# Kernel optimization log

Hardware: AMD Instinct MI355X
Metric: run time of the kernel (lower is better)

## Reference

```python
import jax, jax.numpy as jnp
from jax import lax
import numpy as np

B = 4096
L = 20  # nb_latents


def conv2d(x, w, b, stride, pad):
    y = lax.conv_general_dilated(x, w, (stride, stride), [(pad, pad), (pad, pad)],
                                 dimension_numbers=('NCHW', 'OIHW', 'NCHW'))
    return y + b[None, :, None, None]


def deconv2d(x, w, b, stride, pad):
    # w has PyTorch ConvTranspose2d layout [Cin, Cout, kh, kw]
    k = w.shape[2]
    w2 = jnp.flip(w, (2, 3)).transpose(1, 0, 2, 3)  # -> [Cout, Cin, kh, kw]
    y = lax.conv_general_dilated(x, w2, (1, 1), [(k - 1 - pad,) * 2] * 2,
                                 lhs_dilation=(stride, stride),
                                 dimension_numbers=('NCHW', 'OIHW', 'NCHW'))
    return y + b[None, :, None, None]


def setup_inputs() -> dict:
    key = jax.random.key(0)
    ks = jax.random.split(key, 16)

    def W(k, shape, fan_in, scale=1.0):
        return (jax.random.normal(k, shape, jnp.float32) * (scale / np.sqrt(fan_in))).astype(jnp.float32)

    z = lambda n: jnp.zeros((n,), jnp.float32)
    return {
        'x': jax.random.uniform(ks[0], (B, 1, 28, 28), jnp.float32),
        'eps': jax.random.normal(ks[1], (B, L), jnp.float32),
        'w_c1': W(ks[2], (32, 1, 4, 4), 16), 'b_c1': z(32),
        'w_c2': W(ks[3], (32, 32, 4, 4), 512), 'b_c2': z(32),
        'w_c3': W(ks[4], (64, 32, 3, 3), 288), 'b_c3': z(64),
        'w_fc1': W(ks[5], (256, 1024), 1024), 'b_fc1': z(256),
        'w_mu': W(ks[6], (L, 256), 256), 'b_mu': z(L),
        # small scale + negative bias keeps the 100-step exp(logvar) recursion in fp32 range
        'w_ls': W(ks[7], (L, 256), 256, 0.1), 'b_ls': jnp.full((L,), -2.0, jnp.float32),
        'w_fc2': W(ks[8], (256, L), L), 'b_fc2': z(256),
        'w_fc3': W(ks[9], (1024, 256), 256), 'b_fc3': z(1024),
        'w_d1': W(ks[10], (64, 32, 3, 3), 576), 'b_d1': z(32),
        'w_d2': W(ks[11], (32, 32, 4, 4), 512), 'b_d2': z(32),
        'w_d3': W(ks[12], (32, 1, 4, 4), 512), 'b_d3': z(1),
    }


def reference(x, eps, w_c1, b_c1, w_c2, b_c2, w_c3, b_c3, w_fc1, b_fc1,
              w_mu, b_mu, w_ls, b_ls, w_fc2, b_fc2, w_fc3, b_fc3,
              w_d1, b_d1, w_d2, b_d2, w_d3, b_d3):
    # ---- encoder ----
    h = jax.nn.relu(conv2d(x, w_c1, b_c1, 2, 1))   # [B,32,14,14]
    h = jax.nn.relu(conv2d(h, w_c2, b_c2, 2, 1))   # [B,32,7,7]
    h = jax.nn.relu(conv2d(h, w_c3, b_c3, 2, 1))   # [B,64,4,4]
    h = jax.nn.relu(h.reshape(-1, 64 * 4 * 4) @ w_fc1.T + b_fc1)
    mu = h @ w_mu.T + b_mu          # [B,L]
    logvar = h @ w_ls.T + b_ls      # [B,L]

    # ---- reversing: 100 gradient-ascent steps on KLD (eval-mode reparameterize) ----
    # KLD = -0.5 * sum(1 + ls - mu^2 - exp(ls))  =>  dKLD/dmu = mu, dKLD/dls = 0.5*(exp(ls)-1)
    lr = 0.1
    def step(c, _):
        m, s = c
        return (m + lr * m, s + lr * 0.5 * (jnp.exp(s) - 1.0)), None
    (mu_r, ls_r), _ = lax.scan(step, (mu, logvar), None, length=100)
    zlat = eps * jnp.exp(0.5 * ls_r) + mu_r

    # ---- decoder ----
    d = jax.nn.relu(zlat @ w_fc2.T + b_fc2)
    d = jax.nn.relu(d @ w_fc3.T + b_fc3).reshape(-1, 64, 4, 4)
    d = jax.nn.relu(deconv2d(d, w_d1, b_d1, 2, 1))       # [B,32,7,7]
    d = jax.nn.relu(deconv2d(d, w_d2, b_d2, 2, 1))       # [B,32,14,14]
    x_hat = jax.nn.sigmoid(deconv2d(d, w_d3, b_d3, 2, 1))  # [B,1,28,28]
    return x_hat, mu, logvar
```

## Files before the change

### kernel.cpp

```cpp
#include <hip/hip_runtime.h>
#include <math.h>

#define BATCH 4096

__device__ __forceinline__ void dot4a(float& acc, const float4 v, const float4 wt) {
    acc = fmaf(v.x, wt.x, acc);
    acc = fmaf(v.y, wt.y, acc);
    acc = fmaf(v.z, wt.z, acc);
    acc = fmaf(v.w, wt.w, acc);
}

__global__ __launch_bounds__(256) void tr_kernel(
    const float* __restrict__ w_c2, const float* __restrict__ w_c3,
    const float* __restrict__ w_d1, const float* __restrict__ w_d2,
    const float* __restrict__ w_d3,
    float* __restrict__ wt2, float* __restrict__ wt3,
    float* __restrict__ wtd1, float* __restrict__ wtd2, float* __restrict__ wtd3)
{
    int i = blockIdx.x * 256 + threadIdx.x;
    if (i < 16384) {
        int ci = i & 31, tap = (i >> 5) & 15, co = i >> 9;
        wt2[i] = w_c2[(co * 32 + ci) * 16 + tap];
    }
    if (i < 18432) {
        int ci = i & 31, r = i >> 5, tap = r % 9, co = r / 9;
        wt3[i] = w_c3[(co * 32 + ci) * 9 + tap];
    }
    if (i < 18432) {
        int ci = i & 63, r = i >> 6, tap = r % 9, co = r / 9;
        wtd1[i] = w_d1[(ci * 32 + co) * 9 + tap];
    }
    if (i < 16384) {
        int ci = i & 31, tap = (i >> 5) & 15, co = i >> 9;
        wtd2[i] = w_d2[(ci * 32 + co) * 16 + tap];
    }
    if (i < 512) {
        int ci = i & 31, tap = i >> 5;
        wtd3[i] = w_d3[ci * 16 + tap];
    }
}

__global__ __launch_bounds__(256, 3) void enc_kernel(
    const float* __restrict__ x,
    const float* __restrict__ w_c1, const float* __restrict__ b_c1,
    const float* __restrict__ wt2, const float* __restrict__ b_c2,
    const float* __restrict__ wt3, const float* __restrict__ b_c3,
    float* __restrict__ h3out)
{
    __shared__ __align__(16) float buf[12708];
    float* s_h1 = buf;
    float* s_h3 = buf;
    float* s_x  = buf + 9216;
    float* s_h2 = buf + 10116;

    const int n = blockIdx.x, tid = threadIdx.x;
    const int wv = __builtin_amdgcn_readfirstlane((int)(tid >> 6));
    const int lane = tid & 63;
    const int co0 = wv * 8;

    {
        float4* z1 = (float4*)buf;
        #pragma unroll
        for (int i = tid; i < 2304; i += 256) z1[i] = make_float4(0.f, 0.f, 0.f, 0.f);
        float4* z2 = (float4*)(buf + 10116);
        for (int i = tid; i < 648; i += 256) z2[i] = make_float4(0.f, 0.f, 0.f, 0.f);
        for (int i = tid; i < 30; i += 256) { s_x[i] = 0.f; s_x[870 + i] = 0.f; }
        for (int i = tid; i < 28; i += 256) { s_x[(i + 1) * 30] = 0.f; s_x[(i + 1) * 30 + 29] = 0.f; }
        for (int i = tid; i < 784; i += 256) {
            int iy = i / 28, ix = i - iy * 28;
            s_x[(iy + 1) * 30 + ix + 1] = x[(size_t)n * 784 + i];
        }
    }
    __syncthreads();

    {
        const int poff = lane & 15, pr = lane >> 4;
        const int ca = co0 + pr * 2;
        float w1a[16], w1b[16];
        #pragma unroll
        for (int k = 0; k < 4; ++k) {
            *(float4*)&w1a[4 * k] = *(const float4*)(w_c1 + ca * 16 + 4 * k);
            *(float4*)&w1b[4 * k] = *(const float4*)(w_c1 + (ca + 1) * 16 + 4 * k);
        }
        const float ba = b_c1[ca], bb = b_c1[ca + 1];
        for (int t = 0; t < 13; ++t) {
            int pos = poff + 16 * t;
            bool val = pos < 196;
            int p = val ? pos : 0;
            int oy = p / 14, ox = p - oy * 14;
            const float* bp = s_x + (2 * oy) * 30 + 2 * ox;
            float a0 = ba, a1 = bb;
            #pragma unroll
            for (int ky = 0; ky < 4; ++ky)
                #pragma unroll
                for (int kx = 0; kx < 4; ++kx) {
                    float v = bp[ky * 30 + kx];
                    a0 = fmaf(v, w1a[ky * 4 + kx], a0);
                    a1 = fmaf(v, w1b[ky * 4 + kx], a1);
                }
            if (val)
                *(float2*)(s_h1 + ((oy + 1) * 16 + ox + 1) * 36 + ca) =
                    make_float2(fmaxf(a0, 0.f), fmaxf(a1, 0.f));
        }
    }
    __syncthreads();

    {
        const int parity = lane & 1, pr = (lane >> 1) & 3, cig = lane >> 3;
        const int ca = co0 + pr * 2;
        float4 w2a[16], w2b[16];
        #pragma unroll
        for (int t = 0; t < 16; ++t) {
            w2a[t] = *(const float4*)(wt2 + (ca * 16 + t) * 32 + cig * 4);
            w2b[t] = *(const float4*)(wt2 + ((ca + 1) * 16 + t) * 32 + cig * 4);
        }
        const float ba = b_c2[ca], bb = b_c2[ca + 1];
        for (int t = 0; t < 25; ++t) {
            int pos = parity + 2 * t;
            bool val = pos < 49;
            int p = val ? pos : 0;
            int oy = p / 7, ox = p - oy * 7;
            const float* bp = s_h1 + ((2 * oy) * 16 + 2 * ox) * 36 + cig * 4;
            float a0 = 0.f, a1 = 0.f;
            #pragma unroll
            for (int ky = 0; ky < 4; ++ky)
                #pragma unroll
                for (int kx = 0; kx < 4; ++kx) {
                    float4 v = *(const float4*)(bp + (ky * 16 + kx) * 36);
                    dot4a(a0, v, w2a[ky * 4 + kx]);
                    dot4a(a1, v, w2b[ky * 4 + kx]);
                }
            a0 += __shfl_xor(a0, 8);  a1 += __shfl_xor(a1, 8);
            a0 += __shfl_xor(a0, 16); a1 += __shfl_xor(a1, 16);
            a0 += __shfl_xor(a0, 32); a1 += __shfl_xor(a1, 32);
            if (cig == 0 && val)
                *(float2*)(s_h2 + ((oy + 1) * 9 + ox + 1) * 32 + ca) =
                    make_float2(fmaxf(a0 + ba, 0.f), fmaxf(a1 + bb, 0.f));
        }
    }
    __syncthreads();

    {
        const int pr = lane & 7, cig = lane >> 3;
        const int ca = wv * 16 + pr * 2;
        float4 w3a[9], w3b[9];
        #pragma unroll
        for (int t = 0; t < 9; ++t) {
            w3a[t] = *(const float4*)(wt3 + (ca * 9 + t) * 32 + cig * 4);
            w3b[t] = *(const float4*)(wt3 + ((ca + 1) * 9 + t) * 32 + cig * 4);
        }
        const float ba = b_c3[ca], bb = b_c3[ca + 1];
        #pragma unroll 2
        for (int pos = 0; pos < 16; ++pos) {
            int oy = pos >> 2, ox = pos & 3;
            const float* bp = s_h2 + ((2 * oy) * 9 + 2 * ox) * 32 + cig * 4;
            float a0 = 0.f, a1 = 0.f;
            #pragma unroll
            for (int ky = 0; ky < 3; ++ky)
                #pragma unroll
                for (int kx = 0; kx < 3; ++kx) {
                    float4 v = *(const float4*)(bp + (ky * 9 + kx) * 32);
                    dot4a(a0, v, w3a[ky * 3 + kx]);
                    dot4a(a1, v, w3b[ky * 3 + kx]);
                }
            a0 += __shfl_xor(a0, 8);  a1 += __shfl_xor(a1, 8);
            a0 += __shfl_xor(a0, 16); a1 += __shfl_xor(a1, 16);
            a0 += __shfl_xor(a0, 32); a1 += __shfl_xor(a1, 32);
            if (cig == 0) {
                s_h3[ca * 16 + pos] = fmaxf(a0 + ba, 0.f);
                s_h3[(ca + 1) * 16 + pos] = fmaxf(a1 + bb, 0.f);
            }
        }
    }
    __syncthreads();
    for (int i = tid; i < 1024; i += 256) h3out[(size_t)n * 1024 + i] = s_h3[i];
}

template <bool RELU>
__global__ __launch_bounds__(256) void gemm_nt(
    const float* __restrict__ A, const float* __restrict__ W,
    const float* __restrict__ bias, float* __restrict__ C,
    int M, int N, int K)
{
    __shared__ float As[16][65];
    __shared__ float Ws[16][65];
    const int tid = threadIdx.x;
    const int col0 = blockIdx.x * 64;
    const int row0 = blockIdx.y * 64;
    const int tx = tid & 15, ty = tid >> 4;
    const int lr = tid >> 2, lc = (tid & 3) * 4;
    float acc[4][4] = {};

    for (int k0 = 0; k0 < K; k0 += 16) {
        float4 av = *(const float4*)(A + (size_t)(row0 + lr) * K + k0 + lc);
        float4 wv = *(const float4*)(W + (size_t)(col0 + lr) * K + k0 + lc);
        As[lc + 0][lr] = av.x; As[lc + 1][lr] = av.y; As[lc + 2][lr] = av.z; As[lc + 3][lr] = av.w;
        Ws[lc + 0][lr] = wv.x; Ws[lc + 1][lr] = wv.y; Ws[lc + 2][lr] = wv.z; Ws[lc + 3][lr] = wv.w;
        __syncthreads();
        #pragma unroll
        for (int kk = 0; kk < 16; ++kk) {
            float a[4], b[4];
            #pragma unroll
            for (int i = 0; i < 4; ++i) a[i] = As[kk][ty * 4 + i];
            #pragma unroll
            for (int j = 0; j < 4; ++j) b[j] = Ws[kk][tx * 4 + j];
            #pragma unroll
            for (int i = 0; i < 4; ++i)
                #pragma unroll
                for (int j = 0; j < 4; ++j)
                    acc[i][j] = fmaf(a[i], b[j], acc[i][j]);
        }
        __syncthreads();
    }
    #pragma unroll
    for (int i = 0; i < 4; ++i) {
        int row = row0 + ty * 4 + i;
        float* cp = C + (size_t)row * N + col0 + tx * 4;
        float4 v;
        v.x = acc[i][0] + bias[col0 + tx * 4 + 0];
        v.y = acc[i][1] + bias[col0 + tx * 4 + 1];
        v.z = acc[i][2] + bias[col0 + tx * 4 + 2];
        v.w = acc[i][3] + bias[col0 + tx * 4 + 3];
        if (RELU) {
            v.x = fmaxf(v.x, 0.f); v.y = fmaxf(v.y, 0.f);
            v.z = fmaxf(v.z, 0.f); v.w = fmaxf(v.w, 0.f);
        }
        *(float4*)cp = v;
    }
}

__global__ __launch_bounds__(256) void muls_kernel(
    const float* __restrict__ h,
    const float* __restrict__ w_mu, const float* __restrict__ b_mu,
    const float* __restrict__ w_ls, const float* __restrict__ b_ls,
    float* __restrict__ mu_out, float* __restrict__ ls_out)
{
    int idx = blockIdx.x * 256 + threadIdx.x;
    if (idx >= BATCH * 40) return;
    int i = idx / 40, j = idx % 40;
    bool is_mu = j < 20;
    int jj = is_mu ? j : j - 20;
    const float* wrow = is_mu ? (w_mu + jj * 256) : (w_ls + jj * 256);
    float acc = is_mu ? b_mu[jj] : b_ls[jj];
    const float4* hp = (const float4*)(h + (size_t)i * 256);
    const float4* wp = (const float4*)wrow;
    #pragma unroll 8
    for (int k = 0; k < 64; ++k) {
        float4 hv = hp[k], wv = wp[k];
        acc = fmaf(hv.x, wv.x, acc);
        acc = fmaf(hv.y, wv.y, acc);
        acc = fmaf(hv.z, wv.z, acc);
        acc = fmaf(hv.w, wv.w, acc);
    }
    (is_mu ? mu_out : ls_out)[i * 20 + jj] = acc;
}

__global__ __launch_bounds__(256) void rev_kernel(
    const float* __restrict__ mu, const float* __restrict__ ls,
    const float* __restrict__ eps, float* __restrict__ z)
{
    int idx = blockIdx.x * 256 + threadIdx.x;
    if (idx >= BATCH * 20) return;
    double m = (double)mu[idx];
    double s = (double)ls[idx];
    #pragma unroll 4
    for (int t = 0; t < 100; ++t) {
        m += 0.1 * m;
        s += 0.05 * (exp(s) - 1.0);
    }
    z[idx] = (float)((double)eps[idx] * exp(0.5 * s) + m);
}

__global__ __launch_bounds__(256) void fc2_kernel(
    const float* __restrict__ z, const float* __restrict__ w, const float* __restrict__ b,
    float* __restrict__ out)
{
    int idx = blockIdx.x * 256 + threadIdx.x;
    int i = idx >> 8, j = idx & 255;
    float acc = b[j];
    const float* zp = z + i * 20;
    const float* wp = w + j * 20;
    #pragma unroll
    for (int k = 0; k < 20; ++k) acc = fmaf(zp[k], wp[k], acc);
    out[idx] = fmaxf(acc, 0.f);
}

__global__ __launch_bounds__(256, 3) void dec_kernel(
    const float* __restrict__ hin,
    const float* __restrict__ wtd1, const float* __restrict__ b_d1,
    const float* __restrict__ wtd2, const float* __restrict__ b_d2,
    const float* __restrict__ wtd3, const float* __restrict__ b_d3,
    float* __restrict__ xhat)
{
    __shared__ __align__(16) float dbuf[12896];
    float* s_d2   = dbuf;
    float* s_d1   = dbuf + 9216;
    float* s_in   = dbuf + 11808;
    float* s_part = dbuf + 11808;

    const int n = blockIdx.x, tid = threadIdx.x;
    const int wv = __builtin_amdgcn_readfirstlane((int)(tid >> 6));
    const int lane = tid & 63;
    const int co0 = wv * 8;

    {
        float4* z1 = (float4*)dbuf;
        #pragma unroll
        for (int i = tid; i < 2952; i += 256) z1[i] = make_float4(0.f, 0.f, 0.f, 0.f);
        for (int t = tid; t < 1024; t += 256) {
            int c = t & 63, p = t >> 6;
            s_in[p * 68 + c] = hin[(size_t)n * 1024 + c * 16 + p];
        }
    }
    __syncthreads();

    {
        const int pr = lane & 3, cig = lane >> 2;
        const int ca = co0 + pr * 2;
        float4 wa[9], wb[9];
        #pragma unroll
        for (int t = 0; t < 9; ++t) {
            wa[t] = *(const float4*)(wtd1 + (ca * 9 + t) * 64 + cig * 4);
            wb[t] = *(const float4*)(wtd1 + ((ca + 1) * 9 + t) * 64 + cig * 4);
        }
        const float ba = b_d1[ca], bb = b_d1[ca + 1];
        #pragma unroll
        for (int py = 0; py < 2; ++py) {
            #pragma unroll
            for (int px = 0; px < 2; ++px) {
                const int ny = 4 - py, nx = 4 - px;
                for (int sy = 0; sy < ny; ++sy) {
                    for (int sx = 0; sx < nx; ++sx) {
                        float a0 = 0.f, a1 = 0.f;
                        #pragma unroll
                        for (int a = 0; a <= 1; ++a) {
                            if (a == 1 && py == 0) continue;
                            int ky = py ? (a ? 2 : 0) : 1;
                            int iy = py ? (a ? sy : sy + 1) : sy;
                            #pragma unroll
                            for (int b = 0; b <= 1; ++b) {
                                if (b == 1 && px == 0) continue;
                                int kx = px ? (b ? 2 : 0) : 1;
                                int ix = px ? (b ? sx : sx + 1) : sx;
                                float4 v = *(const float4*)(s_in + (iy * 4 + ix) * 68 + cig * 4);
                                int tp = ky * 3 + kx;
                                dot4a(a0, v, wa[tp]);
                                dot4a(a1, v, wb[tp]);
                            }
                        }
                        a0 += __shfl_xor(a0, 4);  a1 += __shfl_xor(a1, 4);
                        a0 += __shfl_xor(a0, 8);  a1 += __shfl_xor(a1, 8);
                        a0 += __shfl_xor(a0, 16); a1 += __shfl_xor(a1, 16);
                        a0 += __shfl_xor(a0, 32); a1 += __shfl_xor(a1, 32);
                        if (cig == 0) {
                            int oy = 2 * sy + py, ox = 2 * sx + px;
                            *(float2*)(s_d1 + ((oy + 1) * 9 + ox + 1) * 32 + ca) =
                                make_float2(fmaxf(a0 + ba, 0.f), fmaxf(a1 + bb, 0.f));
                        }
                    }
                }
            }
        }
    }
    __syncthreads();

    {
        const int soff = lane & 1, pr = (lane >> 1) & 3, cig = lane >> 3;
        const int ca = co0 + pr * 2;
        float4 wa[16], wb[16];
        #pragma unroll
        for (int t = 0; t < 16; ++t) {
            wa[t] = *(const float4*)(wtd2 + (ca * 16 + t) * 32 + cig * 4);
            wb[t] = *(const float4*)(wtd2 + ((ca + 1) * 16 + t) * 32 + cig * 4);
        }
        const float ba = b_d2[ca], bb = b_d2[ca + 1];
        for (int t = 0; t < 25; ++t) {
            int spos = soff + 2 * t;
            bool val = spos < 49;
            int sp = val ? spos : 0;
            int sy = sp / 7, sx = sp - sy * 7;
            const float* bp = s_d1 + (sy * 9 + sx) * 32 + cig * 4;
            #pragma unroll
            for (int py = 0; py < 2; ++py) {
                float4 va[2][3];
                #pragma unroll
                for (int l = 0; l < 2; ++l)
                    #pragma unroll
                    for (int b = 0; b < 3; ++b)
                        va[l][b] = *(const float4*)(bp + ((l + py) * 9 + b) * 32);
                #pragma unroll
                for (int px = 0; px < 2; ++px) {
                    float a0 = 0.f, a1 = 0.f;
                    #pragma unroll
                    for (int a2 = 0; a2 < 2; ++a2) {
                        int ky = py ? (a2 ? 2 : 0) : (a2 ? 3 : 1);
                        int l = 1 - a2;
                        #pragma unroll
                        for (int b2 = 0; b2 < 2; ++b2) {
                            int kx = px ? (b2 ? 2 : 0) : (b2 ? 3 : 1);
                            int m = px ? (2 - b2) : (1 - b2);
                            int tp = ky * 4 + kx;
                            float4 v = va[l][m];
                            dot4a(a0, v, wa[tp]);
                            dot4a(a1, v, wb[tp]);
                        }
                    }
                    a0 += __shfl_xor(a0, 8);  a1 += __shfl_xor(a1, 8);
                    a0 += __shfl_xor(a0, 16); a1 += __shfl_xor(a1, 16);
                    a0 += __shfl_xor(a0, 32); a1 += __shfl_xor(a1, 32);
                    if (cig == 0 && val) {
                        int oy = 2 * sy + py, ox = 2 * sx + px;
                        *(float2*)(s_d2 + ((oy + 1) * 16 + ox + 1) * 36 + ca) =
                            make_float2(fmaxf(a0 + ba, 0.f), fmaxf(a1 + bb, 0.f));
                    }
                }
            }
        }
    }
    __syncthreads();

    {
        const int ci0 = wv * 8;
        const float bd3 = b_d3[0];
        #pragma unroll
        for (int py = 0; py < 2; ++py) {
            #pragma unroll
            for (int px = 0; px < 2; ++px) {
                float w3r[2][2][8];
                #pragma unroll
                for (int a = 0; a < 2; ++a) {
                    int ky = py ? (a ? 2 : 0) : (a ? 3 : 1);
                    #pragma unroll
                    for (int b = 0; b < 2; ++b) {
                        int kx = px ? (b ? 2 : 0) : (b ? 3 : 1);
                        *(float4*)(w3r[a][b])     = *(const float4*)(wtd3 + (ky * 4 + kx) * 32 + ci0);
                        *(float4*)(w3r[a][b] + 4) = *(const float4*)(wtd3 + (ky * 4 + kx) * 32 + ci0 + 4);
                    }
                }
                for (int t = 0; t < 4; ++t) {
                    int spos = t * 64 + lane;
                    bool val = spos < 196;
                    int sp = val ? spos : 0;
                    int sy = sp / 14, sx = sp - sy * 14;
                    const float* bp = s_d2 + ((sy + py) * 16 + sx + px) * 36 + ci0;
                    float acc = 0.f;
                    #pragma unroll
                    for (int a = 0; a < 2; ++a) {
                        #pragma unroll
                        for (int b = 0; b < 2; ++b) {
                            const float* vp = bp + ((1 - a) * 16 + (1 - b)) * 36;
                            float4 v0 = *(const float4*)(vp);
                            float4 v1 = *(const float4*)(vp + 4);
                            acc = fmaf(v0.x, w3r[a][b][0], acc);
                            acc = fmaf(v0.y, w3r[a][b][1], acc);
                            acc = fmaf(v0.z, w3r[a][b][2], acc);
                            acc = fmaf(v0.w, w3r[a][b][3], acc);
                            acc = fmaf(v1.x, w3r[a][b][4], acc);
                            acc = fmaf(v1.y, w3r[a][b][5], acc);
                            acc = fmaf(v1.z, w3r[a][b][6], acc);
                            acc = fmaf(v1.w, w3r[a][b][7], acc);
                        }
                    }
                    if (val) s_part[wv * 196 + sp] = acc;
                }
                __syncthreads();
                if (tid < 196) {
                    float s = s_part[tid] + s_part[196 + tid] + s_part[392 + tid] + s_part[588 + tid];
                    int sy = tid / 14, sx = tid - sy * 14;
                    xhat[(size_t)n * 784 + (2 * sy + py) * 28 + 2 * sx + px] =
                        1.f / (1.f + expf(-(s + bd3)));
                }
                __syncthreads();
            }
        }
    }
}

extern "C" void kernel_launch(void* const* d_in, const int* in_sizes, int n_in,
                              void* d_out, int out_size, void* d_ws, size_t ws_size,
                              hipStream_t stream) {
    const float* x     = (const float*)d_in[0];
    const float* eps   = (const float*)d_in[1];
    const float* w_c1  = (const float*)d_in[2];
    const float* b_c1  = (const float*)d_in[3];
    const float* w_c2  = (const float*)d_in[4];
    const float* b_c2  = (const float*)d_in[5];
    const float* w_c3  = (const float*)d_in[6];
    const float* b_c3  = (const float*)d_in[7];
    const float* w_fc1 = (const float*)d_in[8];
    const float* b_fc1 = (const float*)d_in[9];
    const float* w_mu  = (const float*)d_in[10];
    const float* b_mu  = (const float*)d_in[11];
    const float* w_ls  = (const float*)d_in[12];
    const float* b_ls  = (const float*)d_in[13];
    const float* w_fc2 = (const float*)d_in[14];
    const float* b_fc2 = (const float*)d_in[15];
    const float* w_fc3 = (const float*)d_in[16];
    const float* b_fc3 = (const float*)d_in[17];
    const float* w_d1  = (const float*)d_in[18];
    const float* b_d1  = (const float*)d_in[19];
    const float* w_d2  = (const float*)d_in[20];
    const float* b_d2  = (const float*)d_in[21];
    const float* w_d3  = (const float*)d_in[22];
    const float* b_d3  = (const float*)d_in[23];

    float* out = (float*)d_out;
    float* x_hat  = out;
    float* mu_out = out + 4096 * 784;
    float* ls_out = mu_out + 4096 * 20;

    float* buf1 = (float*)d_ws;
    float* buf2 = buf1 + 4096 * 1024;
    float* zlat = buf1;
    float* wt2  = buf2 + 4096 * 256;
    float* wt3  = wt2 + 16384;
    float* wtd1 = wt3 + 18432;
    float* wtd2 = wtd1 + 18432;
    float* wtd3 = wtd2 + 16384;

    tr_kernel<<<72, 256, 0, stream>>>(w_c2, w_c3, w_d1, w_d2, w_d3, wt2, wt3, wtd1, wtd2, wtd3);
    enc_kernel<<<BATCH, 256, 0, stream>>>(x, w_c1, b_c1, wt2, b_c2, wt3, b_c3, buf1);
    gemm_nt<true><<<dim3(256 / 64, BATCH / 64), 256, 0, stream>>>(buf1, w_fc1, b_fc1, buf2, BATCH, 256, 1024);
    muls_kernel<<<(BATCH * 40) / 256, 256, 0, stream>>>(buf2, w_mu, b_mu, w_ls, b_ls, mu_out, ls_out);
    rev_kernel<<<(BATCH * 20) / 256, 256, 0, stream>>>(mu_out, ls_out, eps, zlat);
    fc2_kernel<<<BATCH, 256, 0, stream>>>(zlat, w_fc2, b_fc2, buf2);
    gemm_nt<true><<<dim3(1024 / 64, BATCH / 64), 256, 0, stream>>>(buf2, w_fc3, b_fc3, buf1, BATCH, 1024, 256);
    dec_kernel<<<BATCH, 256, 0, stream>>>(buf1, wtd1, b_d1, wtd2, b_d2, wtd3, b_d3, x_hat);
}
```

Before: 787.7 us.

## Fuse mu/logvar projection with reversal loop and restructure decoder deconvolutions

Merges the mu/logvar matvec and the 100-step reversal recursion into one kernel, and moves the logvar recursion from double to float exp. The decoder is reorganised: deconv1/deconv2 assign 4 output channels per lane with fewer shuffle reductions and register-held weights. The final deconv is split into a per-pixel 32-to-16-tap partial product followed by a gather-sum with sigmoid, which removes the per-phase barriers. Float exp in the recursion may change numerics slightly, and the larger per-lane weight arrays raise register pressure.

```diff
diff --git a/kernel.cpp b/kernel.cpp
--- a/kernel.cpp
+++ b/kernel.cpp
@@ -229,46 +229,38 @@
     }
 }
 
-__global__ __launch_bounds__(256) void muls_kernel(
+__global__ __launch_bounds__(256) void mulsrev_kernel(
     const float* __restrict__ h,
     const float* __restrict__ w_mu, const float* __restrict__ b_mu,
     const float* __restrict__ w_ls, const float* __restrict__ b_ls,
-    float* __restrict__ mu_out, float* __restrict__ ls_out)
-{
-    int idx = blockIdx.x * 256 + threadIdx.x;
-    if (idx >= BATCH * 40) return;
-    int i = idx / 40, j = idx % 40;
-    bool is_mu = j < 20;
-    int jj = is_mu ? j : j - 20;
-    const float* wrow = is_mu ? (w_mu + jj * 256) : (w_ls + jj * 256);
-    float acc = is_mu ? b_mu[jj] : b_ls[jj];
-    const float4* hp = (const float4*)(h + (size_t)i * 256);
-    const float4* wp = (const float4*)wrow;
-    #pragma unroll 8
-    for (int k = 0; k < 64; ++k) {
-        float4 hv = hp[k], wv = wp[k];
-        acc = fmaf(hv.x, wv.x, acc);
-        acc = fmaf(hv.y, wv.y, acc);
-        acc = fmaf(hv.z, wv.z, acc);
-        acc = fmaf(hv.w, wv.w, acc);
-    }
-    (is_mu ? mu_out : ls_out)[i * 20 + jj] = acc;
-}
-
-__global__ __launch_bounds__(256) void rev_kernel(
-    const float* __restrict__ mu, const float* __restrict__ ls,
-    const float* __restrict__ eps, float* __restrict__ z)
+    const float* __restrict__ eps,
+    float* __restrict__ mu_out, float* __restrict__ ls_out, float* __restrict__ z)
 {
     int idx = blockIdx.x * 256 + threadIdx.x;
     if (idx >= BATCH * 20) return;
-    double m = (double)mu[idx];
-    double s = (double)ls[idx];
+    int i = idx / 20, j = idx - i * 20;
+    const float4* hp = (const float4*)(h + (size_t)i * 256);
+    const float4* mp = (const float4*)(w_mu + j * 256);
+    const float4* lp = (const float4*)(w_ls + j * 256);
+    float am = b_mu[j], al = b_ls[j];
+    #pragma unroll 8
+    for (int k = 0; k < 64; ++k) {
+        float4 hv = hp[k], mv = mp[k], lv = lp[k];
+        am = fmaf(hv.x, mv.x, am); al = fmaf(hv.x, lv.x, al);
+        am = fmaf(hv.y, mv.y, am); al = fmaf(hv.y, lv.y, al);
+        am = fmaf(hv.z, mv.z, am); al = fmaf(hv.z, lv.z, al);
+        am = fmaf(hv.w, mv.w, am); al = fmaf(hv.w, lv.w, al);
+    }
+    mu_out[idx] = am;
+    ls_out[idx] = al;
+    double m = (double)am;
+    float s = al;
     #pragma unroll 4
     for (int t = 0; t < 100; ++t) {
         m += 0.1 * m;
-        s += 0.05 * (exp(s) - 1.0);
-    }
-    z[idx] = (float)((double)eps[idx] * exp(0.5 * s) + m);
+        s += 0.05f * (expf(s) - 1.f);
+    }
+    z[idx] = fmaf(eps[idx], expf(0.5f * s), (float)m);
 }
 
 __global__ __launch_bounds__(256) void fc2_kernel(
@@ -292,11 +284,11 @@
     const float* __restrict__ wtd3, const float* __restrict__ b_d3,
     float* __restrict__ xhat)
 {
-    __shared__ __align__(16) float dbuf[12896];
-    float* s_d2   = dbuf;
-    float* s_d1   = dbuf + 9216;
-    float* s_in   = dbuf + 11808;
-    float* s_part = dbuf + 11808;
+    __shared__ __align__(16) float dbuf[11060];
+    float* s_d2 = dbuf;
+    float* s_d1 = dbuf + 7056;
+    float* s_in = dbuf + 9972;
+    float* sP   = dbuf + 7056;
 
     const int n = blockIdx.x, tid = threadIdx.x;
     const int wv = __builtin_amdgcn_readfirstlane((int)(tid >> 6));
@@ -304,9 +296,8 @@
     const int co0 = wv * 8;
 
     {
-        float4* z1 = (float4*)dbuf;
-        #pragma unroll
-        for (int i = tid; i < 2952; i += 256) z1[i] = make_float4(0.f, 0.f, 0.f, 0.f);
+        float4* z1 = (float4*)(dbuf + 7056);
+        for (int i = tid; i < 729; i += 256) z1[i] = make_float4(0.f, 0.f, 0.f, 0.f);
         for (int t = tid; t < 1024; t += 256) {
             int c = t & 63, p = t >> 6;
             s_in[p * 68 + c] = hin[(size_t)n * 1024 + c * 16 + p];
@@ -315,162 +306,194 @@
     __syncthreads();
 
     {
-        const int pr = lane & 3, cig = lane >> 2;
-        const int ca = co0 + pr * 2;
-        float4 wa[9], wb[9];
-        #pragma unroll
-        for (int t = 0; t < 9; ++t) {
-            wa[t] = *(const float4*)(wtd1 + (ca * 9 + t) * 64 + cig * 4);
-            wb[t] = *(const float4*)(wtd1 + ((ca + 1) * 9 + t) * 64 + cig * 4);
-        }
-        const float ba = b_d1[ca], bb = b_d1[ca + 1];
+        const int cig = lane & 7, pq = (lane >> 3) & 1, poff = lane >> 4;
+        const int ci0 = cig * 8;
+        const int ca = co0 + pq * 4;
+        float bd[4];
+        #pragma unroll
+        for (int u = 0; u < 4; ++u) bd[u] = b_d1[ca + u];
+
         #pragma unroll
         for (int py = 0; py < 2; ++py) {
             #pragma unroll
             for (int px = 0; px < 2; ++px) {
                 const int ny = 4 - py, nx = 4 - px;
-                for (int sy = 0; sy < ny; ++sy) {
-                    for (int sx = 0; sx < nx; ++sx) {
-                        float a0 = 0.f, a1 = 0.f;
+                const int P = ny * nx;
+                const int na = py ? 2 : 1, nb = px ? 2 : 1;
+                float4 wd[4][2][2][2];
+                #pragma unroll
+                for (int u = 0; u < 4; ++u)
+                    #pragma unroll
+                    for (int a = 0; a < 2; ++a) {
+                        if (a >= na) continue;
                         #pragma unroll
-                        for (int a = 0; a <= 1; ++a) {
-                            if (a == 1 && py == 0) continue;
+                        for (int b = 0; b < 2; ++b) {
+                            if (b >= nb) continue;
                             int ky = py ? (a ? 2 : 0) : 1;
-                            int iy = py ? (a ? sy : sy + 1) : sy;
+                            int kx = px ? (b ? 2 : 0) : 1;
+                            const float* wp = wtd1 + ((ca + u) * 9 + ky * 3 + kx) * 64 + ci0;
+                            wd[u][a][b][0] = *(const float4*)(wp);
+                            wd[u][a][b][1] = *(const float4*)(wp + 4);
+                        }
+                    }
+                const int niter = (P + 3) >> 2;
+                for (int it = 0; it < niter; ++it) {
+                    int pidx = it * 4 + poff;
+                    bool act = pidx < P;
+                    int p = act ? pidx : 0;
+                    int sy = p / nx, sx = p - sy * nx;
+                    float acc[4] = {};
+                    #pragma unroll
+                    for (int a = 0; a < 2; ++a) {
+                        if (a >= na) continue;
+                        int iy = py ? (a ? sy : sy + 1) : sy;
+                        #pragma unroll
+                        for (int b = 0; b < 2; ++b) {
+                            if (b >= nb) continue;
+                            int ix = px ? (b ? sx : sx + 1) : sx;
+                            const float* bp = s_in + (iy * 4 + ix) * 68 + ci0;
+                            float4 v0 = *(const float4*)(bp);
+                            float4 v1 = *(const float4*)(bp + 4);
                             #pragma unroll
-                            for (int b = 0; b <= 1; ++b) {
-                                if (b == 1 && px == 0) continue;
-                                int kx = px ? (b ? 2 : 0) : 1;
-                                int ix = px ? (b ? sx : sx + 1) : sx;
-                                float4 v = *(const float4*)(s_in + (iy * 4 + ix) * 68 + cig * 4);
-                                int tp = ky * 3 + kx;
-                                dot4a(a0, v, wa[tp]);
-                                dot4a(a1, v, wb[tp]);
+                            for (int u = 0; u < 4; ++u) {
+                                dot4a(acc[u], v0, wd[u][a][b][0]);
+                                dot4a(acc[u], v1, wd[u][a][b][1]);
                             }
                         }
-                        a0 += __shfl_xor(a0, 4);  a1 += __shfl_xor(a1, 4);
-                        a0 += __shfl_xor(a0, 8);  a1 += __shfl_xor(a1, 8);
-                        a0 += __shfl_xor(a0, 16); a1 += __shfl_xor(a1, 16);
-                        a0 += __shfl_xor(a0, 32); a1 += __shfl_xor(a1, 32);
-                        if (cig == 0) {
-                            int oy = 2 * sy + py, ox = 2 * sx + px;
-                            *(float2*)(s_d1 + ((oy + 1) * 9 + ox + 1) * 32 + ca) =
-                                make_float2(fmaxf(a0 + ba, 0.f), fmaxf(a1 + bb, 0.f));
-                        }
                     }
-                }
-            }
-        }
-    }
-    __syncthreads();
-
-    {
-        const int soff = lane & 1, pr = (lane >> 1) & 3, cig = lane >> 3;
-        const int ca = co0 + pr * 2;
-        float4 wa[16], wb[16];
-        #pragma unroll
-        for (int t = 0; t < 16; ++t) {
-            wa[t] = *(const float4*)(wtd2 + (ca * 16 + t) * 32 + cig * 4);
-            wb[t] = *(const float4*)(wtd2 + ((ca + 1) * 16 + t) * 32 + cig * 4);
-        }
-        const float ba = b_d2[ca], bb = b_d2[ca + 1];
-        for (int t = 0; t < 25; ++t) {
-            int spos = soff + 2 * t;
-            bool val = spos < 49;
-            int sp = val ? spos : 0;
+                    #pragma unroll
+                    for (int u = 0; u < 4; ++u) {
+                        acc[u] += __shfl_xor(acc[u], 1);
+                        acc[u] += __shfl_xor(acc[u], 2);
+                        acc[u] += __shfl_xor(acc[u], 4);
+                    }
+                    if (cig == 0 && act) {
+                        int oy = 2 * sy + py, ox = 2 * sx + px;
+                        float4 o;
+                        o.x = fmaxf(acc[0] + bd[0], 0.f);
+                        o.y = fmaxf(acc[1] + bd[1], 0.f);
+                        o.z = fmaxf(acc[2] + bd[2], 0.f);
+                        o.w = fmaxf(acc[3] + bd[3], 0.f);
+                        *(float4*)(s_d1 + ((oy + 1) * 9 + ox + 1) * 36 + ca) = o;
+                    }
+                }
+            }
+        }
+    }
+    __syncthreads();
+
+    {
+        const int cig = lane & 3, pq = (lane >> 2) & 1;
+        const int py = (lane >> 3) & 1, px = (lane >> 4) & 1, poff = lane >> 5;
+        const int ci0 = cig * 8;
+        const int ca = co0 + pq * 4;
+        float4 w2[4][2][2][2];
+        float bd[4];
+        #pragma unroll
+        for (int u = 0; u < 4; ++u) {
+            bd[u] = b_d2[ca + u];
+            #pragma unroll
+            for (int a = 0; a < 2; ++a)
+                #pragma unroll
+                for (int b = 0; b < 2; ++b) {
+                    int ky = py ? (a ? 2 : 0) : (a ? 3 : 1);
+                    int kx = px ? (b ? 2 : 0) : (b ? 3 : 1);
+                    const float* wp = wtd2 + ((ca + u) * 16 + ky * 4 + kx) * 32 + ci0;
+                    w2[u][a][b][0] = *(const float4*)(wp);
+                    w2[u][a][b][1] = *(const float4*)(wp + 4);
+                }
+        }
+        for (int it = 0; it < 25; ++it) {
+            int pidx = it * 2 + poff;
+            bool act = pidx < 49;
+            int sp = act ? pidx : 0;
             int sy = sp / 7, sx = sp - sy * 7;
-            const float* bp = s_d1 + (sy * 9 + sx) * 32 + cig * 4;
-            #pragma unroll
-            for (int py = 0; py < 2; ++py) {
-                float4 va[2][3];
-                #pragma unroll
-                for (int l = 0; l < 2; ++l)
+            float acc[4] = {};
+            #pragma unroll
+            for (int a = 0; a < 2; ++a) {
+                int iy = py ? (a ? sy : sy + 1) : (a ? sy - 1 : sy);
+                #pragma unroll
+                for (int b = 0; b < 2; ++b) {
+                    int ix = px ? (b ? sx : sx + 1) : (b ? sx - 1 : sx);
+                    const float* bp = s_d1 + ((iy + 1) * 9 + ix + 1) * 36 + ci0;
+                    float4 v0 = *(const float4*)(bp);
+                    float4 v1 = *(const float4*)(bp + 4);
                     #pragma unroll
-                    for (int b = 0; b < 3; ++b)
-                        va[l][b] = *(const float4*)(bp + ((l + py) * 9 + b) * 32);
-                #pragma unroll
-                for (int px = 0; px < 2; ++px) {
-                    float a0 = 0.f, a1 = 0.f;
+                    for (int u = 0; u < 4; ++u) {
+                        dot4a(acc[u], v0, w2[u][a][b][0]);
+                        dot4a(acc[u], v1, w2[u][a][b][1]);
+                    }
+                }
+            }
+            #pragma unroll
+            for (int u = 0; u < 4; ++u) {
+                acc[u] += __shfl_xor(acc[u], 1);
+                acc[u] += __shfl_xor(acc[u], 2);
+            }
+            if (cig == 0 && act) {
+                int oy = 2 * sy + py, ox = 2 * sx + px;
+                float4 o;
+                o.x = fmaxf(acc[0] + bd[0], 0.f);
+                o.y = fmaxf(acc[1] + bd[1], 0.f);
+                o.z = fmaxf(acc[2] + bd[2], 0.f);
+                o.w = fmaxf(acc[3] + bd[3], 0.f);
+                *(float4*)(s_d2 + (oy * 14 + ox) * 36 + ca) = o;
+            }
+        }
+    }
+    __syncthreads();
+
+    {
+        const int pp = lane & 15, tq = lane >> 4;
+        float4 w3[4][8];
+        #pragma unroll
+        for (int j = 0; j < 4; ++j)
+            #pragma unroll
+            for (int q = 0; q < 8; ++q)
+                w3[j][q] = *(const float4*)(wtd3 + (tq * 4 + j) * 32 + q * 4);
+        #pragma unroll
+        for (int r = 0; r < 4; ++r) {
+            int p = r * 64 + wv * 16 + pp;
+            if (p < 196) {
+                const float* bp = s_d2 + p * 36;
+                float4 v[8];
+                #pragma unroll
+                for (int q = 0; q < 8; ++q) v[q] = *(const float4*)(bp + q * 4);
+                #pragma unroll
+                for (int j = 0; j < 4; ++j) {
+                    float acc = 0.f;
                     #pragma unroll
-                    for (int a2 = 0; a2 < 2; ++a2) {
-                        int ky = py ? (a2 ? 2 : 0) : (a2 ? 3 : 1);
-                        int l = 1 - a2;
-                        #pragma unroll
-                        for (int b2 = 0; b2 < 2; ++b2) {
-                            int kx = px ? (b2 ? 2 : 0) : (b2 ? 3 : 1);
-                            int m = px ? (2 - b2) : (1 - b2);
-                            int tp = ky * 4 + kx;
-                            float4 v = va[l][m];
-                            dot4a(a0, v, wa[tp]);
-                            dot4a(a1, v, wb[tp]);
-                        }
-                    }
-                    a0 += __shfl_xor(a0, 8);  a1 += __shfl_xor(a1, 8);
-                    a0 += __shfl_xor(a0, 16); a1 += __shfl_xor(a1, 16);
-                    a0 += __shfl_xor(a0, 32); a1 += __shfl_xor(a1, 32);
-                    if (cig == 0 && val) {
-                        int oy = 2 * sy + py, ox = 2 * sx + px;
-                        *(float2*)(s_d2 + ((oy + 1) * 16 + ox + 1) * 36 + ca) =
-                            make_float2(fmaxf(a0 + ba, 0.f), fmaxf(a1 + bb, 0.f));
-                    }
-                }
-            }
-        }
-    }
-    __syncthreads();
-
-    {
-        const int ci0 = wv * 8;
+                    for (int q = 0; q < 8; ++q) dot4a(acc, v[q], w3[j][q]);
+                    sP[(tq * 4 + j) * 196 + p] = acc;
+                }
+            }
+        }
+    }
+    __syncthreads();
+
+    {
         const float bd3 = b_d3[0];
         #pragma unroll
-        for (int py = 0; py < 2; ++py) {
-            #pragma unroll
-            for (int px = 0; px < 2; ++px) {
-                float w3r[2][2][8];
+        for (int t = 0; t < 4; ++t) {
+            int o = t * 256 + tid;
+            if (o < 784) {
+                int oy = o / 28, ox = o - oy * 28;
+                int py = oy & 1, px = ox & 1, sy = oy >> 1, sx = ox >> 1;
+                float acc = bd3;
                 #pragma unroll
                 for (int a = 0; a < 2; ++a) {
                     int ky = py ? (a ? 2 : 0) : (a ? 3 : 1);
+                    int iy = py ? (a ? sy : sy + 1) : (a ? sy - 1 : sy);
+                    bool vy = (unsigned)iy < 14u;
                     #pragma unroll
                     for (int b = 0; b < 2; ++b) {
                         int kx = px ? (b ? 2 : 0) : (b ? 3 : 1);
-                        *(float4*)(w3r[a][b])     = *(const float4*)(wtd3 + (ky * 4 + kx) * 32 + ci0);
-                        *(float4*)(w3r[a][b] + 4) = *(const float4*)(wtd3 + (ky * 4 + kx) * 32 + ci0 + 4);
+                        int ix = px ? (b ? sx : sx + 1) : (b ? sx - 1 : sx);
+                        if (vy && (unsigned)ix < 14u)
+                            acc += sP[(ky * 4 + kx) * 196 + iy * 14 + ix];
                     }
                 }
-                for (int t = 0; t < 4; ++t) {
-                    int spos = t * 64 + lane;
-                    bool val = spos < 196;
-                    int sp = val ? spos : 0;
-                    int sy = sp / 14, sx = sp - sy * 14;
-                    const float* bp = s_d2 + ((sy + py) * 16 + sx + px) * 36 + ci0;
-                    float acc = 0.f;
-                    #pragma unroll
-                    for (int a = 0; a < 2; ++a) {
-                        #pragma unroll
-                        for (int b = 0; b < 2; ++b) {
-                            const float* vp = bp + ((1 - a) * 16 + (1 - b)) * 36;
-                            float4 v0 = *(const float4*)(vp);
-                            float4 v1 = *(const float4*)(vp + 4);
-                            acc = fmaf(v0.x, w3r[a][b][0], acc);
-                            acc = fmaf(v0.y, w3r[a][b][1], acc);
-                            acc = fmaf(v0.z, w3r[a][b][2], acc);
-                            acc = fmaf(v0.w, w3r[a][b][3], acc);
-                            acc = fmaf(v1.x, w3r[a][b][4], acc);
-                            acc = fmaf(v1.y, w3r[a][b][5], acc);
-                            acc = fmaf(v1.z, w3r[a][b][6], acc);
-                            acc = fmaf(v1.w, w3r[a][b][7], acc);
-                        }
-                    }
-                    if (val) s_part[wv * 196 + sp] = acc;
-                }
-                __syncthreads();
-                if (tid < 196) {
-                    float s = s_part[tid] + s_part[196 + tid] + s_part[392 + tid] + s_part[588 + tid];
-                    int sy = tid / 14, sx = tid - sy * 14;
-                    xhat[(size_t)n * 784 + (2 * sy + py) * 28 + 2 * sx + px] =
-                        1.f / (1.f + expf(-(s + bd3)));
-                }
-                __syncthreads();
+                xhat[(size_t)n * 784 + o] = 1.f / (1.f + expf(-acc));
             }
         }
     }
@@ -521,8 +544,7 @@
     tr_kernel<<<72, 256, 0, stream>>>(w_c2, w_c3, w_d1, w_d2, w_d3, wt2, wt3, wtd1, wtd2, wtd3);
     enc_kernel<<<BATCH, 256, 0, stream>>>(x, w_c1, b_c1, wt2, b_c2, wt3, b_c3, buf1);
     gemm_nt<true><<<dim3(256 / 64, BATCH / 64), 256, 0, stream>>>(buf1, w_fc1, b_fc1, buf2, BATCH, 256, 1024);
-    muls_kernel<<<(BATCH * 40) / 256, 256, 0, stream>>>(buf2, w_mu, b_mu, w_ls, b_ls, mu_out, ls_out);
-    rev_kernel<<<(BATCH * 20) / 256, 256, 0, stream>>>(mu_out, ls_out, eps, zlat);
+    mulsrev_kernel<<<(BATCH * 20) / 256, 256, 0, stream>>>(buf2, w_mu, b_mu, w_ls, b_ls, eps, mu_out, ls_out, zlat);
     fc2_kernel<<<BATCH, 256, 0, stream>>>(zlat, w_fc2, b_fc2, buf2);
     gemm_nt<true><<<dim3(1024 / 64, BATCH / 64), 256, 0, stream>>>(buf2, w_fc3, b_fc3, buf1, BATCH, 1024, 256);
     dec_kernel<<<BATCH, 256, 0, stream>>>(buf1, wtd1, b_d1, wtd2, b_d2, wtd3, b_d3, x_hat);
```

New measurement: 648.8 us. -17.6%, faster.
